# Kernel tuning notes

Measured on AMD Instinct MI355X. Metric: run time of the kernel, lower is better.

Reference implementation:

```python
import jax, jax.numpy as jnp
import numpy as np

CUTOFFS = [2000, 10000, 50000]
HIDDEN = 1024
BATCH = 2048


def setup_inputs() -> dict:
    key = jax.random.key(0)
    ks = jax.random.split(key, 8)
    s = 1.0 / np.sqrt(HIDDEN)
    return {
        "hidden": jax.random.normal(ks[0], (BATCH, HIDDEN), dtype=jnp.float32),
        "target": jax.random.randint(ks[1], (BATCH,), 0, CUTOFFS[-1]),
        # head weight: candidates[:cutoffs[0]] plus 2 tail vectors, transposed -> (hidden, 2002)
        "head_w": jax.random.normal(ks[2], (HIDDEN, CUTOFFS[0] + 2), dtype=jnp.float32) * s,
        # tail 0 (cluster [2000,10000), size 8000): down 1024->1024 (rf^0), decode 1024->8000
        "down0": jax.random.normal(ks[3], (HIDDEN, HIDDEN), dtype=jnp.float32) * s,
        "dec0": jax.random.normal(ks[4], (HIDDEN, CUTOFFS[1] - CUTOFFS[0]), dtype=jnp.float32) * s,
        # tail 1 (cluster [10000,50000), size 40000): down 1024->256 (rf^1), decode 256->40000
        "down1": jax.random.normal(ks[5], (HIDDEN, HIDDEN // 4), dtype=jnp.float32) * s,
        "dec1": jax.random.normal(ks[6], (HIDDEN // 4, CUTOFFS[2] - CUTOFFS[1]), dtype=jnp.float32) * s,
    }


def reference(hidden, target, head_w, down0, dec0, down1, dec1):
    # Head logits over first bucket + one pseudo-token per tail cluster.
    head = hidden @ head_w  # (B, 2002)
    # Cluster membership masks (fixed shapes instead of data-dependent gather;
    # rows outside a cluster produce zeroed logits, matching index_select semantics
    # up to padding).
    m0 = ((target >= CUTOFFS[0]) & (target < CUTOFFS[1])).astype(hidden.dtype)
    m1 = ((target >= CUTOFFS[1]) & (target < CUTOFFS[2])).astype(hidden.dtype)
    # Grouped small matmuls: down-project then decode per tail cluster.
    t0 = ((hidden @ down0) @ dec0) * m0[:, None]  # (B, 8000)
    t1 = ((hidden @ down1) @ dec1) * m1[:, None]  # (B, 40000)
    return jnp.concatenate([head, t0, t1], axis=1)  # (B, 50002)
```

## Files before the change

kernel.cpp:

```cpp
#include <hip/hip_runtime.h>

typedef unsigned short u16;
typedef unsigned int   u32;
typedef __attribute__((ext_vector_type(4))) float  f32x4;
typedef __attribute__((ext_vector_type(8))) __bf16 bf16x8;
typedef __attribute__((ext_vector_type(8))) u16    u16x8;
typedef __attribute__((address_space(1))) void as1_void;
typedef __attribute__((address_space(3))) void as3_void;

__device__ int g_idx0[2048];
__device__ int g_idx1[2048];
__device__ int g_cnt[2];

__device__ __forceinline__ void async16(const void* g, void* l) {
  __builtin_amdgcn_global_load_lds((const as1_void*)g, (as3_void*)l, 16, 0, 0);
}

__device__ __forceinline__ u16 f2bf(float f) {
  u32 u = __builtin_bit_cast(u32, f);
  return (u16)((u + 0x7fffu + ((u >> 16) & 1u)) >> 16);
}

template <int MODE>
__device__ __forceinline__ void gemm_core(
    u16* As, u16* Bs,
    const u16* __restrict__ A, const u16* __restrict__ Bt,
    void* __restrict__ Cout, int K, int ldc, int colOff, int Nreal,
    const int* __restrict__ idx, int cnt, int bm, int bn)
{
  const int tid  = threadIdx.x;
  const int wid  = tid >> 6;
  const int lane = tid & 63;
  const int quad = lane >> 4;
  const int l16  = lane & 15;
  const int wm = (wid >> 1) * 64;
  const int wn = (wid & 1) * 64;

  f32x4 acc[4][4] = {};

  const int srow = wid * 16 + (lane >> 2);
  const int scol = (lane & 3) * 8;

  size_t ar0, ar1;
  if (MODE == 1) { ar0 = (size_t)idx[bm + srow]; ar1 = (size_t)idx[bm + srow + 64]; }
  else           { ar0 = (size_t)(bm + srow);    ar1 = ar0 + 64; }
  const u16* ga0 = A + ar0 * K + scol;
  const u16* ga1 = A + ar1 * K + scol;
  const u16* gb0 = Bt + (size_t)(bn + srow) * K + scol;
  const u16* gb1 = gb0 + (size_t)64 * K;

  for (int k0 = 0; k0 < K; k0 += 32) {
    async16(ga0 + k0, As + wid * 512);
    async16(ga1 + k0, As + wid * 512 + 2048);
    async16(gb0 + k0, Bs + wid * 512);
    async16(gb1 + k0, Bs + wid * 512 + 2048);
    __syncthreads();

    bf16x8 af[4], bfr[4];
#pragma unroll
    for (int i = 0; i < 4; i++) {
      af[i]  = *reinterpret_cast<const bf16x8*>(As + (wm + i * 16 + l16) * 32 + quad * 8);
      bfr[i] = *reinterpret_cast<const bf16x8*>(Bs + (wn + i * 16 + l16) * 32 + quad * 8);
    }
#pragma unroll
    for (int mi = 0; mi < 4; mi++)
#pragma unroll
      for (int ni = 0; ni < 4; ni++)
        acc[mi][ni] = __builtin_amdgcn_mfma_f32_16x16x32_bf16(af[mi], bfr[ni], acc[mi][ni], 0, 0, 0);
    __syncthreads();
  }

#pragma unroll
  for (int mi = 0; mi < 4; mi++) {
    const int rbase = bm + wm + mi * 16 + quad * 4;
    int  orow[4];
    bool vld[4];
#pragma unroll
    for (int r = 0; r < 4; r++) {
      if (MODE == 2) {
        int slot = rbase + r;
        vld[r]  = slot < cnt;
        orow[r] = vld[r] ? idx[slot] : 0;
      } else {
        vld[r] = true; orow[r] = rbase + r;
      }
    }
#pragma unroll
    for (int ni = 0; ni < 4; ni++) {
      const int col = bn + wn + ni * 16 + l16;
      if (MODE == 1) {
        u16* C = (u16*)Cout;
#pragma unroll
        for (int r = 0; r < 4; r++)
          C[(size_t)orow[r] * ldc + col] = f2bf(acc[mi][ni][r]);
      } else {
        if (col < Nreal) {
          float* C = (float*)Cout;
#pragma unroll
          for (int r = 0; r < 4; r++)
            if (vld[r]) C[(size_t)orow[r] * ldc + colOff + col] = acc[mi][ni][r];
        }
      }
    }
  }
}

__device__ __forceinline__ void tconv_core(float (*tile)[33], const float* __restrict__ in,
                                           u16* __restrict__ out, int K, int N, int bx, int by) {
  int tx = threadIdx.x & 31, ty = threadIdx.x >> 5;
  int n0 = bx * 32, k0 = by * 32;
#pragma unroll
  for (int i = 0; i < 4; i++) {
    int k = k0 + ty + i * 8;
    int n = n0 + tx;
    tile[ty + i * 8][tx] = (n < N) ? in[(size_t)k * N + n] : 0.0f;
  }
  __syncthreads();
#pragma unroll
  for (int i = 0; i < 4; i++)
    out[(size_t)(n0 + ty + i * 8) * K + k0 + tx] = f2bf(tile[tx][ty + i * 8]);
}

__global__ __launch_bounds__(256) void prep(
    const float* __restrict__ hidden, const int* __restrict__ target,
    const float* __restrict__ head_w, const float* __restrict__ down0,
    const float* __restrict__ dec0, const float* __restrict__ down1,
    const float* __restrict__ dec1,
    u16* __restrict__ hA, u16* __restrict__ head_wT, u16* __restrict__ down0T,
    u16* __restrict__ dec0T, u16* __restrict__ down1T, u16* __restrict__ dec1T)
{
  __shared__ float tile[32][33];
  __shared__ int cc[2];
  const int b = blockIdx.x;
  const int tid = threadIdx.x;
  if (b < 1024) {
    int i = b * 256 + tid;
    const float4* p = reinterpret_cast<const float4*>(hidden) + (size_t)i * 2;
    float4 a = p[0], c = p[1];
    u16x8 o;
    o[0] = f2bf(a.x); o[1] = f2bf(a.y); o[2] = f2bf(a.z); o[3] = f2bf(a.w);
    o[4] = f2bf(c.x); o[5] = f2bf(c.y); o[6] = f2bf(c.z); o[7] = f2bf(c.w);
    reinterpret_cast<u16x8*>(hA)[i] = o;
  } else if (b < 3072) {
    int r = b - 1024;  tconv_core(tile, head_w, head_wT, 1024, 2002,  r % 64,   r / 64);
  } else if (b < 4096) {
    int r = b - 3072;  tconv_core(tile, down0,  down0T,  1024, 1024,  r % 32,   r / 32);
  } else if (b < 12160) {
    int r = b - 4096;  tconv_core(tile, dec0,   dec0T,   1024, 8000,  r % 252,  r / 252);
  } else if (b < 12416) {
    int r = b - 12160; tconv_core(tile, down1,  down1T,  1024, 256,   r % 8,    r / 8);
  } else if (b < 22432) {
    int r = b - 12416; tconv_core(tile, dec1,   dec1T,   256,  40000, r % 1252, r / 1252);
  } else {
    if (tid < 2) cc[tid] = 0;
    __syncthreads();
    for (int i = tid; i < 2048; i += 256) {
      int t = target[i];
      if (t >= 2000 && t < 10000)  g_idx0[atomicAdd(&cc[0], 1)] = i;
      else if (t >= 10000)         g_idx1[atomicAdd(&cc[1], 1)] = i;
    }
    __syncthreads();
    int n0 = cc[0], n1 = cc[1];
    for (int i = tid; i < 2048; i += 256) {
      if (i >= n0) g_idx0[i] = 0;
      if (i >= n1) g_idx1[i] = 0;
    }
    if (tid == 0) { g_cnt[0] = n0; g_cnt[1] = n1; }
  }
}

__global__ __launch_bounds__(256, 2) void g1(
    const u16* __restrict__ hA, const u16* __restrict__ head_wT,
    const u16* __restrict__ down0T, const u16* __restrict__ down1T,
    u16* __restrict__ X0c, u16* __restrict__ X1c, float* __restrict__ out)
{
  __shared__ u16 As[4096], Bs[4096];
  const int b = blockIdx.x;
  if (b < 256) {
    gemm_core<0>(As, Bs, hA, head_wT, out, 1024, 50002, 0, 2002,
                 nullptr, 2048, (b >> 4) * 128, (b & 15) * 128);
  } else if (b < 384) {
    int r = b - 256, bm = (r & 15) * 128, bn = (r >> 4) * 128;
    if (bm < g_cnt[0])
      gemm_core<1>(As, Bs, hA, down0T, X0c, 1024, 1024, 0, 1024, g_idx0, g_cnt[0], bm, bn);
  } else {
    int r = b - 384, bm = (r & 15) * 128, bn = (r >> 4) * 128;
    if (bm < g_cnt[1])
      gemm_core<1>(As, Bs, hA, down1T, X1c, 1024, 256, 0, 256, g_idx1, g_cnt[1], bm, bn);
  }
}

__global__ __launch_bounds__(256, 2) void g2(
    const u16* __restrict__ X0c, const u16* __restrict__ X1c,
    const u16* __restrict__ dec0T, const u16* __restrict__ dec1T,
    const int* __restrict__ target, float* __restrict__ out)
{
  __shared__ u16 As[4096], Bs[4096];
  const int b = blockIdx.x;
  if (b < 1008) {
    int bm = (b & 15) * 128, bn = (b >> 4) * 128;
    if (bm < g_cnt[0])
      gemm_core<2>(As, Bs, X0c, dec0T, out, 1024, 50002, 2002, 8000, g_idx0, g_cnt[0], bm, bn);
  } else if (b < 6016) {
    int r = b - 1008, bm = (r & 15) * 128, bn = (r >> 4) * 128;
    if (bm < g_cnt[1])
      gemm_core<2>(As, Bs, X1c, dec1T, out, 256, 50002, 10002, 40000, g_idx1, g_cnt[1], bm, bn);
  } else {
    int row = b - 6016;
    int t = target[row];
    bool in0 = (t >= 2000) && (t < 10000);
    bool in1 = (t >= 10000);
    float2* p = reinterpret_cast<float2*>(out + (size_t)row * 50002);
    float2 z; z.x = 0.0f; z.y = 0.0f;
    if (!in0)
      for (int i = threadIdx.x; i < 4000; i += 256)  p[1001 + i] = z;
    if (!in1)
      for (int i = threadIdx.x; i < 20000; i += 256) p[5001 + i] = z;
  }
}

extern "C" void kernel_launch(void* const* d_in, const int* in_sizes, int n_in,
                              void* d_out, int out_size, void* d_ws, size_t ws_size,
                              hipStream_t stream) {
  const float* hidden = (const float*)d_in[0];
  const int*   target = (const int*)d_in[1];
  const float* head_w = (const float*)d_in[2];
  const float* down0  = (const float*)d_in[3];
  const float* dec0   = (const float*)d_in[4];
  const float* down1  = (const float*)d_in[5];
  const float* dec1   = (const float*)d_in[6];
  float* out = (float*)d_out;

  char* ws = (char*)d_ws;
  const size_t NEED = 53280768;
  if (ws_size < NEED) return;
  u16* hA      = (u16*)(ws);
  u16* head_wT = (u16*)(ws + 4194304);
  u16* down0T  = (u16*)(ws + 8388608);
  u16* dec0T   = (u16*)(ws + 10485760);
  u16* down1T  = (u16*)(ws + 27000832);
  u16* dec1T   = (u16*)(ws + 27525120);
  u16* X0c     = (u16*)(ws + 48037888);
  u16* X1c     = (u16*)(ws + 52232192);

  prep<<<22433, 256, 0, stream>>>(hidden, target, head_w, down0, dec0, down1, dec1,
                                  hA, head_wT, down0T, dec0T, down1T, dec1T);
  g1<<<416, 256, 0, stream>>>(hA, head_wT, down0T, down1T, X0c, X1c, out);
  g2<<<8064, 256, 0, stream>>>(X0c, X1c, dec0T, dec1T, target, out);
}
```

Measured before the change: 603.9 us.

## Overlap decoder weight transposes and mask zeroing with first-stage GEMMs

Moves the large dec0/dec1 transpose-to-bf16 work and the row zero-fill out of separate phases and into the same launch as the head and down-projection GEMMs, so the memory-bound conversion can run alongside the small compute-bound first stage. The prep kernel shrinks to the small conversions and the index build, and the decode GEMMs get their own final kernel. The transpose tile reuses the GEMM's shared A buffer, and block scheduling order may leave GEMM blocks sharing CUs with bandwidth-heavy transpose blocks.

New measurement: 648.4 us. +7.4%, slower.

```diff
diff --git a/kernel.cpp b/kernel.cpp
--- a/kernel.cpp
+++ b/kernel.cpp
@@ -121,13 +121,12 @@
     out[(size_t)(n0 + ty + i * 8) * K + k0 + tx] = f2bf(tile[tx][ty + i * 8]);
 }
 
-__global__ __launch_bounds__(256) void prep(
+__global__ __launch_bounds__(256) void prepA(
     const float* __restrict__ hidden, const int* __restrict__ target,
     const float* __restrict__ head_w, const float* __restrict__ down0,
-    const float* __restrict__ dec0, const float* __restrict__ down1,
-    const float* __restrict__ dec1,
+    const float* __restrict__ down1,
     u16* __restrict__ hA, u16* __restrict__ head_wT, u16* __restrict__ down0T,
-    u16* __restrict__ dec0T, u16* __restrict__ down1T, u16* __restrict__ dec1T)
+    u16* __restrict__ down1T)
 {
   __shared__ float tile[32][33];
   __shared__ int cc[2];
@@ -145,12 +144,8 @@
     int r = b - 1024;  tconv_core(tile, head_w, head_wT, 1024, 2002,  r % 64,   r / 64);
   } else if (b < 4096) {
     int r = b - 3072;  tconv_core(tile, down0,  down0T,  1024, 1024,  r % 32,   r / 32);
-  } else if (b < 12160) {
-    int r = b - 4096;  tconv_core(tile, dec0,   dec0T,   1024, 8000,  r % 252,  r / 252);
-  } else if (b < 12416) {
-    int r = b - 12160; tconv_core(tile, down1,  down1T,  1024, 256,   r % 8,    r / 8);
-  } else if (b < 22432) {
-    int r = b - 12416; tconv_core(tile, dec1,   dec1T,   256,  40000, r % 1252, r / 1252);
+  } else if (b < 4352) {
+    int r = b - 4096;  tconv_core(tile, down1,  down1T,  1024, 256,   r % 8,    r / 8);
   } else {
     if (tid < 2) cc[tid] = 0;
     __syncthreads();
@@ -169,9 +164,12 @@
   }
 }
 
-__global__ __launch_bounds__(256, 2) void g1(
+__global__ __launch_bounds__(256, 2) void gemmA(
     const u16* __restrict__ hA, const u16* __restrict__ head_wT,
     const u16* __restrict__ down0T, const u16* __restrict__ down1T,
+    const float* __restrict__ dec0, const float* __restrict__ dec1,
+    u16* __restrict__ dec0T, u16* __restrict__ dec1T,
+    const int* __restrict__ target,
     u16* __restrict__ X0c, u16* __restrict__ X1c, float* __restrict__ out)
 {
   __shared__ u16 As[4096], Bs[4096];
@@ -183,30 +181,18 @@
     int r = b - 256, bm = (r & 15) * 128, bn = (r >> 4) * 128;
     if (bm < g_cnt[0])
       gemm_core<1>(As, Bs, hA, down0T, X0c, 1024, 1024, 0, 1024, g_idx0, g_cnt[0], bm, bn);
-  } else {
+  } else if (b < 416) {
     int r = b - 384, bm = (r & 15) * 128, bn = (r >> 4) * 128;
     if (bm < g_cnt[1])
       gemm_core<1>(As, Bs, hA, down1T, X1c, 1024, 256, 0, 256, g_idx1, g_cnt[1], bm, bn);
-  }
-}
-
-__global__ __launch_bounds__(256, 2) void g2(
-    const u16* __restrict__ X0c, const u16* __restrict__ X1c,
-    const u16* __restrict__ dec0T, const u16* __restrict__ dec1T,
-    const int* __restrict__ target, float* __restrict__ out)
-{
-  __shared__ u16 As[4096], Bs[4096];
-  const int b = blockIdx.x;
-  if (b < 1008) {
-    int bm = (b & 15) * 128, bn = (b >> 4) * 128;
-    if (bm < g_cnt[0])
-      gemm_core<2>(As, Bs, X0c, dec0T, out, 1024, 50002, 2002, 8000, g_idx0, g_cnt[0], bm, bn);
-  } else if (b < 6016) {
-    int r = b - 1008, bm = (r & 15) * 128, bn = (r >> 4) * 128;
-    if (bm < g_cnt[1])
-      gemm_core<2>(As, Bs, X1c, dec1T, out, 256, 50002, 10002, 40000, g_idx1, g_cnt[1], bm, bn);
+  } else if (b < 8480) {
+    int r = b - 416;
+    tconv_core(reinterpret_cast<float(*)[33]>(As), dec0, dec0T, 1024, 8000, r % 252, r / 252);
+  } else if (b < 18496) {
+    int r = b - 8480;
+    tconv_core(reinterpret_cast<float(*)[33]>(As), dec1, dec1T, 256, 40000, r % 1252, r / 1252);
   } else {
-    int row = b - 6016;
+    int row = b - 18496;
     int t = target[row];
     bool in0 = (t >= 2000) && (t < 10000);
     bool in1 = (t >= 10000);
@@ -216,6 +202,24 @@
       for (int i = threadIdx.x; i < 4000; i += 256)  p[1001 + i] = z;
     if (!in1)
       for (int i = threadIdx.x; i < 20000; i += 256) p[5001 + i] = z;
+  }
+}
+
+__global__ __launch_bounds__(256, 2) void gemmB(
+    const u16* __restrict__ X0c, const u16* __restrict__ X1c,
+    const u16* __restrict__ dec0T, const u16* __restrict__ dec1T,
+    float* __restrict__ out)
+{
+  __shared__ u16 As[4096], Bs[4096];
+  const int b = blockIdx.x;
+  if (b < 1008) {
+    int bm = (b & 15) * 128, bn = (b >> 4) * 128;
+    if (bm < g_cnt[0])
+      gemm_core<2>(As, Bs, X0c, dec0T, out, 1024, 50002, 2002, 8000, g_idx0, g_cnt[0], bm, bn);
+  } else {
+    int r = b - 1008, bm = (r & 15) * 128, bn = (r >> 4) * 128;
+    if (bm < g_cnt[1])
+      gemm_core<2>(As, Bs, X1c, dec1T, out, 256, 50002, 10002, 40000, g_idx1, g_cnt[1], bm, bn);
   }
 }
 
@@ -243,8 +247,9 @@
   u16* X0c     = (u16*)(ws + 48037888);
   u16* X1c     = (u16*)(ws + 52232192);
 
-  prep<<<22433, 256, 0, stream>>>(hidden, target, head_w, down0, dec0, down1, dec1,
-                                  hA, head_wT, down0T, dec0T, down1T, dec1T);
-  g1<<<416, 256, 0, stream>>>(hA, head_wT, down0T, down1T, X0c, X1c, out);
-  g2<<<8064, 256, 0, stream>>>(X0c, X1c, dec0T, dec1T, target, out);
-}
+  prepA<<<4353, 256, 0, stream>>>(hidden, target, head_w, down0, down1,
+                                  hA, head_wT, down0T, down1T);
+  gemmA<<<20544, 256, 0, stream>>>(hA, head_wT, down0T, down1T, dec0, dec1,
+                                   dec0T, dec1T, target, X0c, X1c, out);
+  gemmB<<<6016, 256, 0, stream>>>(X0c, X1c, dec0T, dec1T, out);
+}
```
